# Kernel tuning notes

Measured on AMD Instinct MI355X. Metric: run time of the kernel, lower is better.

## Reference

```python
import jax, jax.numpy as jnp
import numpy as np

DIM = 192
SCALE = DIM ** (-0.5)


def setup_inputs() -> dict:
    key = jax.random.key(0)
    qkv = jax.random.normal(key, (8, 4096, 3 * DIM), dtype=jnp.float32)
    return {"qkv": qkv}


def reference(qkv):
    # qkv: [B, T, 3C] -> q, k, v each [B, T, C]
    q, k, v = jnp.split(qkv, 3, axis=2)
    # scale_in=True: scale q and k before distance computation
    q = q * SCALE
    k = k * SCALE
    # L2-distance attention logits: -||q_t - k_s||_2, computed via the
    # expansion ||q||^2 + ||k||^2 - 2 q.k (same as torch.cdist for large inputs)
    q2 = jnp.sum(q * q, axis=-1)          # [B, T]
    k2 = jnp.sum(k * k, axis=-1)          # [B, S]
    d2 = q2[:, :, None] + k2[:, None, :] - 2.0 * jnp.einsum('btc,bsc->bts', q, k)
    d2 = jnp.maximum(d2, 0.0)
    # safe sqrt (zero distance on the diagonal since q and k come from same tokens)
    dist = jnp.where(d2 > 0, jnp.sqrt(jnp.where(d2 > 0, d2, 1.0)), 0.0)
    attn_logits = -dist                    # [B, T, S]
    attn = jax.nn.softmax(attn_logits, axis=-1)
    return jnp.einsum('bts,bsc->btc', attn, v)  # [B, T, C]
```

## Files before the change

kernel.cpp:

```cpp
#include <hip/hip_runtime.h>
#include <hip/hip_bf16.h>


#define BB 8
#define TT 4096
#define CD 192

typedef __attribute__((ext_vector_type(8))) short short8;
typedef __attribute__((ext_vector_type(4))) float float4v;
typedef __attribute__((ext_vector_type(2))) unsigned int uint2v;

constexpr float A2C = (float)(2.0813689810056077 / 192.0);

static __device__ __forceinline__ unsigned short f2bf(float f) {
  unsigned u = __builtin_bit_cast(unsigned, f);
  unsigned r = u + 0x7fffu + ((u >> 16) & 1u);
  return (unsigned short)(r >> 16);
}
static __device__ __forceinline__ float bf2f(unsigned short b) {
  return __builtin_bit_cast(float, (unsigned)b << 16);
}

__global__ __launch_bounds__(256) void prep(
    const float* __restrict__ qkv, short8* __restrict__ qsw,
    short8* __restrict__ ksw, short8* __restrict__ vsw,
    float* __restrict__ q2, float* __restrict__ k2) {
  __shared__ unsigned short tile[32 * 584];
  const int t = threadIdx.x;
  const int b = blockIdx.x >> 7;
  const int sc = blockIdx.x & 127;
  const float* src = qkv + ((size_t)(b * TT + sc * 32)) * (3 * CD);
#pragma unroll
  for (int j = 0; j < 18; ++j) {
    int f = j * 256 + t;
    int row = f / 144, c4 = (f % 144) * 4;
    float4v x = *(const float4v*)(src + (size_t)row * 576 + c4);
    unsigned r0 = (unsigned)f2bf(x[0]) | ((unsigned)f2bf(x[1]) << 16);
    unsigned r1 = (unsigned)f2bf(x[2]) | ((unsigned)f2bf(x[3]) << 16);
    *(uint2v*)&tile[row * 584 + c4] = (uint2v){r0, r1};
  }
  __syncthreads();

  const int lane = t & 63, w = t >> 6;
  const int L = lane & 15, q = lane >> 4;
  const int which = w >> 1;
  const int s16o = w & 1;
  const int row = s16o * 16 + L;
  short8* dst = which ? ksw : qsw;
  const size_t ubase = ((size_t)(b * 256 + sc * 2 + s16o)) * 6;
  float ss = 0.f;
#pragma unroll
  for (int ch = 0; ch < 6; ++ch) {
    short8 fr = *(const short8*)&tile[row * 584 + which * CD + ch * 32 + q * 8];
#pragma unroll
    for (int j = 0; j < 8; ++j) {
      float f = bf2f((unsigned short)fr[j]);
      ss += f * f;
    }
    dst[(ubase + ch) * 64 + lane] = fr;
  }
  ss += __shfl_xor(ss, 16);
  ss += __shfl_xor(ss, 32);
  if (lane < 16)
    (which ? k2 : q2)[b * TT + sc * 32 + s16o * 16 + lane] = ss * A2C;

#pragma unroll
  for (int i = 0; i < 3; ++i) {
    int nt2 = w * 3 + i;
    short8 fr;
#pragma unroll
    for (int j = 0; j < 8; ++j)
      fr[j] = (short)tile[(q * 8 + j) * 584 + 2 * CD + nt2 * 16 + L];
    vsw[((size_t)(b * 12 + nt2) * 128 + sc) * 64 + lane] = fr;
  }
}

__global__ __launch_bounds__(256, 2) void attn2(
    const short8* __restrict__ qsw, const short8* __restrict__ ksw,
    const short8* __restrict__ vsw, const float* __restrict__ q2,
    const float* __restrict__ k2, float* __restrict__ out) {
  __shared__ __align__(16) unsigned char s_lds[49152 + 9216];
  float* ldsP = (float*)(s_lds + 49152);

  const int tid = threadIdx.x;
  const int w = tid >> 6;
  const int lane = tid & 63;
  const int L = lane & 15;
  const int q = lane >> 4;
  const int b = blockIdx.x & 7;
  const int qt = blockIdx.x >> 3;
  const int q0 = qt * 64 + w * 16;
  const size_t bT = (size_t)b * TT;

  float* pw = ldsP + w * 576;

  auto stage = [&](int itile, int buf) {
    const char* gk = (const char*)(ksw + ((size_t)(b * 256 + 2 * itile)) * 6 * 64);
#pragma unroll
    for (int j = 0; j < 3; ++j) {
      int u = w * 3 + j;
      const char* ga = gk + (u * 64 + lane) * 16;
      char* la = (char*)s_lds + buf * 12288 + u * 1024;
      __builtin_amdgcn_global_load_lds(
          (const __attribute__((address_space(1))) void*)ga,
          (__attribute__((address_space(3))) void*)la, 16, 0, 0);
    }
#pragma unroll
    for (int j = 0; j < 3; ++j) {
      int u = w * 3 + j;
      const char* ga = (const char*)vsw +
                       (((size_t)(b * 12 + u) * 128 + itile) * 64 + lane) * 16;
      char* la = (char*)s_lds + 24576 + buf * 12288 + u * 1024;
      __builtin_amdgcn_global_load_lds(
          (const __attribute__((address_space(1))) void*)ga,
          (__attribute__((address_space(3))) void*)la, 16, 0, 0);
    }
  };

  short8 qf[6];
#pragma unroll
  for (int ch = 0; ch < 6; ++ch)
    qf[ch] = qsw[((size_t)(b * 256 + (q0 >> 4)) * 6 + ch) * 64 + lane];

  float q2l[4];
#pragma unroll
  for (int r = 0; r < 4; ++r) q2l[r] = q2[bT + q0 + 4 * q + r];

  float4v oacc[12];
#pragma unroll
  for (int nt = 0; nt < 12; ++nt) oacc[nt] = (float4v){0.f, 0.f, 0.f, 0.f};
  float lsum[4] = {0.f, 0.f, 0.f, 0.f};

  stage(0, 0);
  __syncthreads();

#pragma unroll 1
  for (int it = 0; it < 128; ++it) {
    const int cur = it & 1;
    if (it + 1 < 128) stage(it + 1, cur ^ 1);
    const int s0 = it * 32;

    float k2l[2];
    k2l[0] = k2[bT + s0 + L];
    k2l[1] = k2[bT + s0 + 16 + L];

    float4v sacc[2];
    sacc[0] = (float4v){0.f, 0.f, 0.f, 0.f};
    sacc[1] = (float4v){0.f, 0.f, 0.f, 0.f};
#pragma unroll
    for (int ch = 0; ch < 6; ++ch) {
      short8 kf0 = *(const short8*)(s_lds + cur * 12288 + ch * 1024 + lane * 16);
      short8 kf1 = *(const short8*)(s_lds + cur * 12288 + (6 + ch) * 1024 + lane * 16);
      sacc[0] = __builtin_amdgcn_mfma_f32_16x16x32_bf16(qf[ch], kf0, sacc[0], 0, 0, 0);
      sacc[1] = __builtin_amdgcn_mfma_f32_16x16x32_bf16(qf[ch], kf1, sacc[1], 0, 0, 0);
    }

    short8 vf[12];
#pragma unroll
    for (int nt = 0; nt < 12; ++nt)
      vf[nt] = *(const short8*)(s_lds + 24576 + cur * 12288 + nt * 1024 + lane * 16);

#pragma unroll
    for (int nt = 0; nt < 2; ++nt)
#pragma unroll
      for (int r = 0; r < 4; ++r) {
        float dot = sacc[nt][r];
        float tt = fmaf(-2.f * A2C, dot, q2l[r] + k2l[nt]);
        float y = fmaxf(tt, 0.f);
        float p = __builtin_amdgcn_exp2f(-__builtin_amdgcn_sqrtf(y));
        lsum[r] += p;
        pw[(4 * q + r) * 36 + nt * 16 + L] = p;
      }
    float4v p0 = *(const float4v*)(pw + L * 36 + q * 8);
    float4v p1 = *(const float4v*)(pw + L * 36 + q * 8 + 4);
    short8 paf;
#pragma unroll
    for (int j = 0; j < 4; ++j) {
      paf[j] = (short)f2bf(p0[j]);
      paf[j + 4] = (short)f2bf(p1[j]);
    }

#pragma unroll
    for (int nt = 0; nt < 12; ++nt)
      oacc[nt] = __builtin_amdgcn_mfma_f32_16x16x32_bf16(paf, vf[nt], oacc[nt], 0, 0, 0);

    __syncthreads();
  }

#pragma unroll
  for (int r = 0; r < 4; ++r) {
    float ls = lsum[r];
#pragma unroll
    for (int m = 1; m < 16; m <<= 1) ls += __shfl_xor(ls, m);
    float linv = 1.f / ls;
#pragma unroll
    for (int nt = 0; nt < 12; ++nt)
      out[(bT + q0 + 4 * q + r) * CD + nt * 16 + L] = oacc[nt][r] * linv;
  }
}

extern "C" void kernel_launch(void* const* d_in, const int* in_sizes, int n_in,
                              void* d_out, int out_size, void* d_ws, size_t ws_size,
                              hipStream_t stream) {
  (void)in_sizes; (void)n_in; (void)out_size; (void)ws_size;
  const float* qkv = (const float*)d_in[0];
  float* out = (float*)d_out;

  short8* qsw = (short8*)d_ws;
  short8* ksw = qsw + (size_t)BB * 256 * 6 * 64;
  short8* vsw = ksw + (size_t)BB * 256 * 6 * 64;
  float* q2 = (float*)(vsw + (size_t)BB * 12 * 128 * 64);
  float* k2 = q2 + (size_t)BB * TT;

  prep<<<BB * 128, 256, 0, stream>>>(qkv, qsw, ksw, vsw, q2, k2);
  attn2<<<BB * 64, 256, 0, stream>>>(qsw, ksw, vsw, q2, k2, out);
}
```

Before: 248.4 us.

## Split key range across two blocks with atomic accumulation and combine pass

The attention kernel now uses 512-thread blocks covering 128 queries, and splits the key sequence into two halves handled by separate blocks. Partial outputs are atomically added into an output buffer zeroed in prep, and partial row sums are stored per half. A new combine kernel then normalizes each output row. This raises the number of waves and the K/V reuse per block, at the cost of float atomics, an extra kernel launch and an extra pass over the output.

```diff
diff --git a/kernel.cpp b/kernel.cpp
--- a/kernel.cpp
+++ b/kernel.cpp
@@ -24,7 +24,16 @@
 __global__ __launch_bounds__(256) void prep(
     const float* __restrict__ qkv, short8* __restrict__ qsw,
     short8* __restrict__ ksw, short8* __restrict__ vsw,
-    float* __restrict__ q2, float* __restrict__ k2) {
+    float* __restrict__ q2, float* __restrict__ k2,
+    float* __restrict__ out) {
+  {
+    float4v* o4 = (float4v*)out;
+    int base = blockIdx.x * 256 + threadIdx.x;
+#pragma unroll
+    for (int j = 0; j < 6; ++j)
+      o4[base + j * 262144] = (float4v){0.f, 0.f, 0.f, 0.f};
+  }
+
   __shared__ unsigned short tile[32 * 584];
   const int t = threadIdx.x;
   const int b = blockIdx.x >> 7;
@@ -75,11 +84,12 @@
   }
 }
 
-__global__ __launch_bounds__(256, 2) void attn2(
+__global__ __launch_bounds__(512, 4) void attnh(
     const short8* __restrict__ qsw, const short8* __restrict__ ksw,
     const short8* __restrict__ vsw, const float* __restrict__ q2,
-    const float* __restrict__ k2, float* __restrict__ out) {
-  __shared__ __align__(16) unsigned char s_lds[49152 + 9216];
+    const float* __restrict__ k2, float* __restrict__ out,
+    float* __restrict__ lpart) {
+  __shared__ __align__(16) unsigned char s_lds[49152 + 18432];
   float* ldsP = (float*)(s_lds + 49152);
 
   const int tid = threadIdx.x;
@@ -88,32 +98,35 @@
   const int L = lane & 15;
   const int q = lane >> 4;
   const int b = blockIdx.x & 7;
-  const int qt = blockIdx.x >> 3;
-  const int q0 = qt * 64 + w * 16;
+  const int qt = (blockIdx.x >> 3) & 31;
+  const int sh = blockIdx.x >> 8;
+  const int q0 = qt * 128 + w * 16;
   const size_t bT = (size_t)b * TT;
+  const int it0 = sh * 64;
 
   float* pw = ldsP + w * 576;
 
   auto stage = [&](int itile, int buf) {
-    const char* gk = (const char*)(ksw + ((size_t)(b * 256 + 2 * itile)) * 6 * 64);
 #pragma unroll
     for (int j = 0; j < 3; ++j) {
       int u = w * 3 + j;
-      const char* ga = gk + (u * 64 + lane) * 16;
-      char* la = (char*)s_lds + buf * 12288 + u * 1024;
-      __builtin_amdgcn_global_load_lds(
-          (const __attribute__((address_space(1))) void*)ga,
-          (__attribute__((address_space(3))) void*)la, 16, 0, 0);
-    }
-#pragma unroll
-    for (int j = 0; j < 3; ++j) {
-      int u = w * 3 + j;
-      const char* ga = (const char*)vsw +
-                       (((size_t)(b * 12 + u) * 128 + itile) * 64 + lane) * 16;
-      char* la = (char*)s_lds + 24576 + buf * 12288 + u * 1024;
-      __builtin_amdgcn_global_load_lds(
-          (const __attribute__((address_space(1))) void*)ga,
-          (__attribute__((address_space(3))) void*)la, 16, 0, 0);
+      if (u < 12) {
+        const char* ga =
+            (const char*)(ksw + ((size_t)(b * 256 + 2 * itile)) * 6 * 64) +
+            (u * 64 + lane) * 16;
+        char* la = (char*)s_lds + buf * 12288 + u * 1024;
+        __builtin_amdgcn_global_load_lds(
+            (const __attribute__((address_space(1))) void*)ga,
+            (__attribute__((address_space(3))) void*)la, 16, 0, 0);
+      } else {
+        int uv = u - 12;
+        const char* ga = (const char*)vsw +
+                         (((size_t)(b * 12 + uv) * 128 + itile) * 64 + lane) * 16;
+        char* la = (char*)s_lds + 24576 + buf * 12288 + uv * 1024;
+        __builtin_amdgcn_global_load_lds(
+            (const __attribute__((address_space(1))) void*)ga,
+            (__attribute__((address_space(3))) void*)la, 16, 0, 0);
+      }
     }
   };
 
@@ -131,14 +144,15 @@
   for (int nt = 0; nt < 12; ++nt) oacc[nt] = (float4v){0.f, 0.f, 0.f, 0.f};
   float lsum[4] = {0.f, 0.f, 0.f, 0.f};
 
-  stage(0, 0);
+  stage(it0, 0);
   __syncthreads();
 
 #pragma unroll 1
-  for (int it = 0; it < 128; ++it) {
+  for (int it = 0; it < 64; ++it) {
     const int cur = it & 1;
-    if (it + 1 < 128) stage(it + 1, cur ^ 1);
-    const int s0 = it * 32;
+    const int gt = it0 + it;
+    if (it + 1 < 64) stage(gt + 1, cur ^ 1);
+    const int s0 = gt * 32;
 
     float k2l[2];
     k2l[0] = k2[bT + s0 + L];
@@ -187,16 +201,28 @@
     __syncthreads();
   }
 
+  float* op = out + (bT + q0) * (size_t)CD;
 #pragma unroll
   for (int r = 0; r < 4; ++r) {
     float ls = lsum[r];
 #pragma unroll
     for (int m = 1; m < 16; m <<= 1) ls += __shfl_xor(ls, m);
-    float linv = 1.f / ls;
+    if (L == 0) lpart[(size_t)sh * (BB * TT) + bT + q0 + 4 * q + r] = ls;
 #pragma unroll
     for (int nt = 0; nt < 12; ++nt)
-      out[(bT + q0 + 4 * q + r) * CD + nt * 16 + L] = oacc[nt][r] * linv;
-  }
+      atomicAdd(&op[(size_t)(4 * q + r) * CD + nt * 16 + L], oacc[nt][r]);
+  }
+}
+
+__global__ __launch_bounds__(256) void combine(
+    float* __restrict__ out, const float* __restrict__ lpart) {
+  const int idx = blockIdx.x * 256 + threadIdx.x;
+  const int row = idx / 48;
+  const float inv = 1.f / (lpart[row] + lpart[BB * TT + row]);
+  float4v a = ((const float4v*)out)[idx];
+#pragma unroll
+  for (int j = 0; j < 4; ++j) a[j] *= inv;
+  ((float4v*)out)[idx] = a;
 }
 
 extern "C" void kernel_launch(void* const* d_in, const int* in_sizes, int n_in,
@@ -211,7 +237,9 @@
   short8* vsw = ksw + (size_t)BB * 256 * 6 * 64;
   float* q2 = (float*)(vsw + (size_t)BB * 12 * 128 * 64);
   float* k2 = q2 + (size_t)BB * TT;
-
-  prep<<<BB * 128, 256, 0, stream>>>(qkv, qsw, ksw, vsw, q2, k2);
-  attn2<<<BB * 64, 256, 0, stream>>>(qsw, ksw, vsw, q2, k2, out);
-}
+  float* lpart = k2 + (size_t)BB * TT;
+
+  prep<<<BB * 128, 256, 0, stream>>>(qkv, qsw, ksw, vsw, q2, k2, out);
+  attnh<<<BB * 64, 512, 0, stream>>>(qsw, ksw, vsw, q2, k2, out, lpart);
+  combine<<<BB * TT * 48 / 256, 256, 0, stream>>>(out, lpart);
+}
```

Result: slower. 520.8 us (+109.6%).
